# Performance work log

Measured on AMD Instinct MI355X. Metric: run time of the kernel, lower is better.

The kernel has to match this reference:

```python
import jax, jax.numpy as jnp
import numpy as np

N_NODES = 50000
HID = 256


def _gcn_norm(edge_index, n_nodes):
    # PyG GCNConv default: add self-loops, symmetric normalization
    src, dst = edge_index[0], edge_index[1]
    loop = jnp.arange(n_nodes, dtype=src.dtype)
    src = jnp.concatenate([src, loop])
    dst = jnp.concatenate([dst, loop])
    deg = jax.ops.segment_sum(jnp.ones_like(src, dtype=jnp.float32), dst, num_segments=n_nodes)
    dinv = jnp.where(deg > 0, jax.lax.rsqrt(jnp.maximum(deg, 1.0)), 0.0)
    norm = dinv[src] * dinv[dst]  # [E + N]
    return src, dst, norm


def _gcn_conv(x, W, b, src, dst, norm, n_nodes):
    h = x @ W                                   # [N, H] dense transform first (PyG order)
    msg = h[src] * norm[:, None]                # gather + scale
    out = jax.ops.segment_sum(msg, dst, num_segments=n_nodes)
    return out + b


def setup_inputs() -> dict:
    key = jax.random.key(0)
    ks = jax.random.split(key, 8)
    x = jax.random.normal(ks[0], (N_NODES, HID), dtype=jnp.float32)
    edge_index = jax.random.randint(ks[1], (2, 1600000), 0, N_NODES, dtype=jnp.int64)
    s = 1.0 / np.sqrt(HID)
    W1 = jax.random.normal(ks[2], (HID, HID), dtype=jnp.float32) * s
    b1 = jnp.zeros((HID,), dtype=jnp.float32)
    Wmu = jax.random.normal(ks[3], (HID, HID), dtype=jnp.float32) * s
    bmu = jnp.zeros((HID,), dtype=jnp.float32)
    Wls = jax.random.normal(ks[4], (HID, HID), dtype=jnp.float32) * s * 0.1
    bls = jnp.zeros((HID,), dtype=jnp.float32)
    return {"x": x, "edge_index": edge_index, "W1": W1, "b1": b1,
            "Wmu": Wmu, "bmu": bmu, "Wls": Wls, "bls": bls}


def reference(x, edge_index, W1, b1, Wmu, bmu, Wls, bls):
    n = x.shape[0]
    src, dst, norm = _gcn_norm(edge_index, n)
    h = jax.nn.relu(_gcn_conv(x, W1, b1, src, dst, norm, n))
    mu = _gcn_conv(h, Wmu, bmu, src, dst, norm, n)
    logstd = _gcn_conv(h, Wls, bls, src, dst, norm, n)
    std = jnp.exp(logstd)
    eps = jax.random.normal(jax.random.key(1), std.shape, dtype=std.dtype)
    z = mu + std * eps
    return (z, mu, logstd)
```

## Files before the change

### kernel.cpp

```cpp
#include <hip/hip_runtime.h>
#include <stdint.h>

#define HID 256

typedef __bf16 bf16x8 __attribute__((ext_vector_type(8)));
typedef float  f32x4  __attribute__((ext_vector_type(4)));
typedef unsigned int uint4v __attribute__((ext_vector_type(4)));

__device__ __forceinline__ unsigned short f2bf(float f){
  unsigned int x = __float_as_uint(f);
  x += 0x7FFFu + ((x >> 16) & 1u);
  return (unsigned short)(x >> 16);
}
__device__ __forceinline__ float bf2f(unsigned int u){
  return __uint_as_float(u << 16);
}
__device__ __forceinline__ float bflo(unsigned int x){ return __uint_as_float(x << 16); }
__device__ __forceinline__ float bfhi(unsigned int x){ return __uint_as_float(x & 0xFFFF0000u); }
__device__ __forceinline__ bf16x8 ntload8(const unsigned short* p){
  uint4v t = __builtin_nontemporal_load((const uint4v*)p);
  return __builtin_bit_cast(bf16x8, t);
}

__global__ void count_kernel(const int* __restrict__ ei, int E, int* __restrict__ deg){
  int e = blockIdx.x*256 + threadIdx.x;
  if (e < E) atomicAdd(&deg[ei[E + e]], 1);
}

__global__ void dinv_kernel(const int* __restrict__ deg, float* __restrict__ dinv, int N){
  int i = blockIdx.x*256 + threadIdx.x;
  if (i < N) dinv[i] = 1.0f / sqrtf((float)(deg[i] + 1));
}

__global__ void scan1_kernel(const int* __restrict__ deg, int* __restrict__ rowptr,
                             int* __restrict__ partials, int N){
  __shared__ int sm[256];
  int t = threadIdx.x;
  int i = blockIdx.x*256 + t;
  int v = (i < N) ? deg[i] : 0;
  int acc = v;
  sm[t] = acc;
  __syncthreads();
  for (int off = 1; off < 256; off <<= 1){
    int add = (t >= off) ? sm[t - off] : 0;
    __syncthreads();
    acc += add;
    sm[t] = acc;
    __syncthreads();
  }
  if (i < N) rowptr[i] = acc - v;
  if (t == 255) partials[blockIdx.x] = acc;
}

__global__ void scan2_kernel(int* __restrict__ partials, int nb){
  __shared__ int sm[256];
  int t = threadIdx.x;
  int v = (t < nb) ? partials[t] : 0;
  int acc = v;
  sm[t] = acc;
  __syncthreads();
  for (int off = 1; off < 256; off <<= 1){
    int add = (t >= off) ? sm[t - off] : 0;
    __syncthreads();
    acc += add;
    sm[t] = acc;
    __syncthreads();
  }
  if (t < nb) partials[t] = acc - v;
}

__global__ void scan3_kernel(int* __restrict__ rowptr, const int* __restrict__ partials,
                             int N, int E){
  int i = blockIdx.x*256 + threadIdx.x;
  if (i < N) rowptr[i] += partials[blockIdx.x];
  if (i == 0) rowptr[N] = E;
}

__global__ void scatter_kernel(const int* __restrict__ ei, int E, const int* __restrict__ rowptr,
                               int* __restrict__ fill, const float* __restrict__ dinv,
                               int* __restrict__ col, float* __restrict__ wgt){
  int e = blockIdx.x*256 + threadIdx.x;
  if (e >= E) return;
  int s = ei[e];
  int d = ei[E + e];
  int p = rowptr[d] + atomicAdd(&fill[d], 1);
  col[p] = s;
  wgt[p] = dinv[s] * dinv[d];
}

__global__ void convX_kernel(const float* __restrict__ x, unsigned short* __restrict__ xb, int total8){
  int t = blockIdx.x*256 + threadIdx.x;
  if (t >= total8) return;
  const float* p = x + (size_t)t*8;
  f32x4 a = *(const f32x4*)p;
  f32x4 b = *(const f32x4*)(p + 4);
  ushort4 o0, o1;
  o0.x = f2bf(a[0]); o0.y = f2bf(a[1]); o0.z = f2bf(a[2]); o0.w = f2bf(a[3]);
  o1.x = f2bf(b[0]); o1.y = f2bf(b[1]); o1.z = f2bf(b[2]); o1.w = f2bf(b[3]);
  ushort4* q = (ushort4*)(xb + (size_t)t*8);
  q[0] = o0; q[1] = o1;
}

__global__ void convW_kernel(const float* __restrict__ W1, const float* __restrict__ Wmu,
                             const float* __restrict__ Wls, unsigned short* __restrict__ Wt){
  int t = blockIdx.x*256 + threadIdx.x;
  if (t >= 3*65536) return;
  int m = t >> 16;
  int r = t & 0xFFFF;
  int n = r >> 8, k = r & 255;
  int ksrc = (m == 0) ? k : ((k & ~63) | ((k & 3) << 4) | ((k >> 2) & 15));
  const float* W = (m == 0) ? W1 : (m == 1 ? Wmu : Wls);
  Wt[t] = f2bf(W[ksrc*HID + n]);
}

__global__ void agg_bf16(const unsigned short* __restrict__ X, unsigned short* __restrict__ Y,
                         const int* __restrict__ rowptr, const int* __restrict__ col,
                         const float* __restrict__ wgt, const float* __restrict__ dinv,
                         int N, int sin, int sout){
  int w = (blockIdx.x * blockDim.x + threadIdx.x) >> 6;
  int lane = threadIdx.x & 63;
  if (w >= N) return;
  int q  = lane >> 4;
  int cl = lane & 15;
  float acc[16];
  #pragma unroll
  for (int k = 0; k < 16; ++k) acc[k] = 0.f;
  int p0 = rowptr[w], p1 = rowptr[w+1];
  for (int base = p0; base < p1; base += 64){
    int idx = base + lane;
    int sc = 0; float wc = 0.f;
    if (idx < p1){ sc = col[idx]; wc = wgt[idx]; }
    int cnt = min(p1 - base, 64);
    for (int j = 0; j < cnt; j += 4){
      int   s = __shfl(sc, j + q);
      float f = __shfl(wc, j + q);
      const unsigned short* rp = X + (size_t)s*sin + cl*16;
      uint4v u0 = *(const uint4v*)rp;
      uint4v u1 = *(const uint4v*)(rp + 8);
      acc[ 0]=fmaf(bflo(u0.x),f,acc[ 0]); acc[ 1]=fmaf(bfhi(u0.x),f,acc[ 1]);
      acc[ 2]=fmaf(bflo(u0.y),f,acc[ 2]); acc[ 3]=fmaf(bfhi(u0.y),f,acc[ 3]);
      acc[ 4]=fmaf(bflo(u0.z),f,acc[ 4]); acc[ 5]=fmaf(bfhi(u0.z),f,acc[ 5]);
      acc[ 6]=fmaf(bflo(u0.w),f,acc[ 6]); acc[ 7]=fmaf(bfhi(u0.w),f,acc[ 7]);
      acc[ 8]=fmaf(bflo(u1.x),f,acc[ 8]); acc[ 9]=fmaf(bfhi(u1.x),f,acc[ 9]);
      acc[10]=fmaf(bflo(u1.y),f,acc[10]); acc[11]=fmaf(bfhi(u1.y),f,acc[11]);
      acc[12]=fmaf(bflo(u1.z),f,acc[12]); acc[13]=fmaf(bfhi(u1.z),f,acc[13]);
      acc[14]=fmaf(bflo(u1.w),f,acc[14]); acc[15]=fmaf(bfhi(u1.w),f,acc[15]);
    }
  }
  #pragma unroll
  for (int k = 0; k < 16; ++k){
    acc[k] += __shfl_xor(acc[k], 16);
    acc[k] += __shfl_xor(acc[k], 32);
  }
  if (q == 0){
    float s2 = dinv[w]; s2 *= s2;
    const unsigned short* rp = X + (size_t)w*sin + cl*16;
    uint4v u0 = *(const uint4v*)rp;
    uint4v u1 = *(const uint4v*)(rp + 8);
    acc[ 0]=fmaf(bflo(u0.x),s2,acc[ 0]); acc[ 1]=fmaf(bfhi(u0.x),s2,acc[ 1]);
    acc[ 2]=fmaf(bflo(u0.y),s2,acc[ 2]); acc[ 3]=fmaf(bfhi(u0.y),s2,acc[ 3]);
    acc[ 4]=fmaf(bflo(u0.z),s2,acc[ 4]); acc[ 5]=fmaf(bfhi(u0.z),s2,acc[ 5]);
    acc[ 6]=fmaf(bflo(u0.w),s2,acc[ 6]); acc[ 7]=fmaf(bfhi(u0.w),s2,acc[ 7]);
    acc[ 8]=fmaf(bflo(u1.x),s2,acc[ 8]); acc[ 9]=fmaf(bfhi(u1.x),s2,acc[ 9]);
    acc[10]=fmaf(bflo(u1.y),s2,acc[10]); acc[11]=fmaf(bfhi(u1.y),s2,acc[11]);
    acc[12]=fmaf(bflo(u1.z),s2,acc[12]); acc[13]=fmaf(bfhi(u1.z),s2,acc[13]);
    acc[14]=fmaf(bflo(u1.w),s2,acc[14]); acc[15]=fmaf(bfhi(u1.w),s2,acc[15]);
    uint4v o0, o1;
    o0.x = (unsigned int)f2bf(acc[ 0]) | ((unsigned int)f2bf(acc[ 1]) << 16);
    o0.y = (unsigned int)f2bf(acc[ 2]) | ((unsigned int)f2bf(acc[ 3]) << 16);
    o0.z = (unsigned int)f2bf(acc[ 4]) | ((unsigned int)f2bf(acc[ 5]) << 16);
    o0.w = (unsigned int)f2bf(acc[ 6]) | ((unsigned int)f2bf(acc[ 7]) << 16);
    o1.x = (unsigned int)f2bf(acc[ 8]) | ((unsigned int)f2bf(acc[ 9]) << 16);
    o1.y = (unsigned int)f2bf(acc[10]) | ((unsigned int)f2bf(acc[11]) << 16);
    o1.z = (unsigned int)f2bf(acc[12]) | ((unsigned int)f2bf(acc[13]) << 16);
    o1.w = (unsigned int)f2bf(acc[14]) | ((unsigned int)f2bf(acc[15]) << 16);
    uint4v* yp = (uint4v*)(Y + (size_t)w*sout + cl*16);
    yp[0] = o0; yp[1] = o1;
  }
}

__global__ __launch_bounds__(256, 8) void gemm1_kernel(const unsigned short* __restrict__ A,
    const unsigned short* __restrict__ Bt, const float* __restrict__ bias,
    unsigned short* __restrict__ H, int N){
  int r0 = blockIdx.x * 32;
  int lane = threadIdx.x & 63;
  int nw = threadIdx.x >> 6;
  int lr = lane & 15, kg = lane >> 4;
  f32x4 acc[2][4] = {};
  for (int ks = 0; ks < 8; ++ks){
    int kb = ks*32 + kg*8;
    bf16x8 af[2];
    #pragma unroll
    for (int rf = 0; rf < 2; ++rf){
      int row = r0 + rf*16 + lr; if (row > N-1) row = N-1;
      af[rf] = *(const bf16x8*)(A + (size_t)row*HID + kb);
    }
    #pragma unroll
    for (int cf = 0; cf < 4; ++cf){
      int c = nw*64 + cf*16 + lr;
      bf16x8 bfr = *(const bf16x8*)(Bt + (size_t)c*HID + kb);
      acc[0][cf] = __builtin_amdgcn_mfma_f32_16x16x32_bf16(af[0], bfr, acc[0][cf], 0, 0, 0);
      acc[1][cf] = __builtin_amdgcn_mfma_f32_16x16x32_bf16(af[1], bfr, acc[1][cf], 0, 0, 0);
    }
  }
  float bv[4];
  #pragma unroll
  for (int cf = 0; cf < 4; ++cf) bv[cf] = bias[nw*64 + cf*16 + lr];
  #pragma unroll
  for (int rf = 0; rf < 2; ++rf){
    #pragma unroll
    for (int i = 0; i < 4; ++i){
      int row = r0 + rf*16 + kg*4 + i;
      if (row < N){
        ushort4 o;
        o.x = f2bf(fmaxf(acc[rf][0][i] + bv[0], 0.0f));
        o.y = f2bf(fmaxf(acc[rf][1][i] + bv[1], 0.0f));
        o.z = f2bf(fmaxf(acc[rf][2][i] + bv[2], 0.0f));
        o.w = f2bf(fmaxf(acc[rf][3][i] + bv[3], 0.0f));
        *(ushort4*)(H + (size_t)row*HID + nw*64 + lr*4) = o;
      }
    }
  }
}

__device__ __forceinline__ unsigned int rotl32(unsigned int v, int r){
  return (v << r) | (v >> (32 - r));
}

__device__ __forceinline__ float gauss_eps(unsigned int idxv){
  unsigned int x0 = 0u, x1 = idxv;
  const unsigned int ks0 = 0u, ks1 = 1u, ks2 = 0x1BD11BDAu ^ 0u ^ 1u;
  x0 += ks0; x1 += ks1;
#define TFR(r) { x0 += x1; x1 = rotl32(x1, r); x1 ^= x0; }
  TFR(13) TFR(15) TFR(26) TFR(6)   x0 += ks1; x1 += ks2 + 1u;
  TFR(17) TFR(29) TFR(16) TFR(24)  x0 += ks2; x1 += ks0 + 2u;
  TFR(13) TFR(15) TFR(26) TFR(6)   x0 += ks0; x1 += ks1 + 3u;
  TFR(17) TFR(29) TFR(16) TFR(24)  x0 += ks1; x1 += ks2 + 4u;
  TFR(13) TFR(15) TFR(26) TFR(6)   x0 += ks2; x1 += ks0 + 5u;
#undef TFR
  unsigned int bits = x0 ^ x1;
  float f = __uint_as_float((bits >> 9) | 0x3F800000u) - 1.0f;
  const float lo = -0.99999994f;
  float u = fmaxf(lo, fmaf(f, 2.0f, lo));
  float t = fmaf(-u, u, 1.0f);
  float wv = -0.69314718056f * __builtin_amdgcn_logf(t);
  float p;
  if (wv < 5.0f){
    wv -= 2.5f;
    p = 2.81022636e-08f;
    p = fmaf(p, wv, 3.43273939e-07f);
    p = fmaf(p, wv, -3.5233877e-06f);
    p = fmaf(p, wv, -4.39150654e-06f);
    p = fmaf(p, wv, 0.00021858087f);
    p = fmaf(p, wv, -0.00125372503f);
    p = fmaf(p, wv, -0.00417768164f);
    p = fmaf(p, wv, 0.246640727f);
    p = fmaf(p, wv, 1.50140941f);
  } else {
    wv = sqrtf(wv) - 3.0f;
    p = -0.000200214257f;
    p = fmaf(p, wv, 0.000100950558f);
    p = fmaf(p, wv, 0.00134934322f);
    p = fmaf(p, wv, -0.00367342844f);
    p = fmaf(p, wv, 0.00573950773f);
    p = fmaf(p, wv, -0.0076224613f);
    p = fmaf(p, wv, 0.00943887047f);
    p = fmaf(p, wv, 1.00167406f);
    p = fmaf(p, wv, 2.83297682f);
  }
  return 1.4142135381698608f * (p * u);
}

__global__ __launch_bounds__(256, 5) void gemm2_kernel(const unsigned short* __restrict__ A2b,
    const unsigned short* __restrict__ Bt, const float* __restrict__ bias,
    float* __restrict__ OUT, int N, int sa){
  __shared__ float sml[16][260];
  int r0 = blockIdx.x * 32;
  int lane = threadIdx.x & 63;
  int nw = threadIdx.x >> 6;
  int lr = lane & 15, kg = lane >> 4;
  f32x4 acc[2][4] = {};
  for (int ks = 0; ks < 8; ++ks){
    int kb = ks*32 + kg*8;
    bf16x8 af[2];
    #pragma unroll
    for (int rf = 0; rf < 2; ++rf){
      int row = r0 + rf*16 + lr; if (row > N-1) row = N-1;
      af[rf] = ntload8(A2b + (size_t)row*sa + kb);
    }
    #pragma unroll
    for (int cf = 0; cf < 4; ++cf){
      int c = nw*64 + cf*16 + lr;
      bf16x8 bfr = *(const bf16x8*)(Bt + (size_t)c*HID + kb);
      acc[0][cf] = __builtin_amdgcn_mfma_f32_16x16x32_bf16(af[0], bfr, acc[0][cf], 0, 0, 0);
      acc[1][cf] = __builtin_amdgcn_mfma_f32_16x16x32_bf16(af[1], bfr, acc[1][cf], 0, 0, 0);
    }
  }
  f32x4 b4 = *(const f32x4*)(bias + lane*4);
  for (int rf = 0; rf < 2; ++rf){
    #pragma unroll
    for (int cf = 0; cf < 4; ++cf){
      int c = nw*64 + cf*16 + lr;
      #pragma unroll
      for (int i = 0; i < 4; ++i) sml[kg*4 + i][c] = acc[rf][cf][i];
    }
    __syncthreads();
    #pragma unroll
    for (int rr = 0; rr < 4; ++rr){
      int rl = nw*4 + rr;
      int row = r0 + rf*16 + rl;
      if (row < N){
        f32x4 m4 = *(const f32x4*)&sml[rl][lane*4];
        m4 += b4;
        __builtin_nontemporal_store(m4, (f32x4*)(OUT + (size_t)row*HID + lane*4));
      }
    }
    __syncthreads();
  }
}

__global__ __launch_bounds__(256, 5) void gemm3_kernel(const unsigned short* __restrict__ A2b,
    const unsigned short* __restrict__ Bt, const float* __restrict__ bias,
    const float* __restrict__ MU, float* __restrict__ Z, float* __restrict__ LS, int N, int sa){
  __shared__ float sml[16][260];
  int r0 = blockIdx.x * 32;
  int lane = threadIdx.x & 63;
  int nw = threadIdx.x >> 6;
  int lr = lane & 15, kg = lane >> 4;
  f32x4 acc[2][4] = {};
  for (int ks = 0; ks < 8; ++ks){
    int kb = ks*32 + kg*8;
    bf16x8 af[2];
    #pragma unroll
    for (int rf = 0; rf < 2; ++rf){
      int row = r0 + rf*16 + lr; if (row > N-1) row = N-1;
      af[rf] = ntload8(A2b + (size_t)row*sa + kb);
    }
    #pragma unroll
    for (int cf = 0; cf < 4; ++cf){
      int c = nw*64 + cf*16 + lr;
      bf16x8 bfr = *(const bf16x8*)(Bt + (size_t)c*HID + kb);
      acc[0][cf] = __builtin_amdgcn_mfma_f32_16x16x32_bf16(af[0], bfr, acc[0][cf], 0, 0, 0);
      acc[1][cf] = __builtin_amdgcn_mfma_f32_16x16x32_bf16(af[1], bfr, acc[1][cf], 0, 0, 0);
    }
  }
  f32x4 b4 = *(const f32x4*)(bias + lane*4);
  for (int rf = 0; rf < 2; ++rf){
    #pragma unroll
    for (int cf = 0; cf < 4; ++cf){
      int c = nw*64 + cf*16 + lr;
      #pragma unroll
      for (int i = 0; i < 4; ++i) sml[kg*4 + i][c] = acc[rf][cf][i];
    }
    __syncthreads();
    #pragma unroll
    for (int rr = 0; rr < 4; ++rr){
      int rl = nw*4 + rr;
      int row = r0 + rf*16 + rl;
      if (row < N){
        size_t base = (size_t)row*HID + lane*4;
        f32x4 l4 = *(const f32x4*)&sml[rl][lane*4];
        l4 += b4;
        f32x4 m4 = *(const f32x4*)(MU + base);
        f32x4 z4;
        #pragma unroll
        for (int j = 0; j < 4; ++j){
          float e = gauss_eps((unsigned int)(base + j));
          float s = __builtin_amdgcn_exp2f(l4[j] * 1.44269504f);
          z4[j] = fmaf(s, e, m4[j]);
        }
        __builtin_nontemporal_store(z4, (f32x4*)(Z  + base));
        __builtin_nontemporal_store(l4, (f32x4*)(LS + base));
      }
    }
    __syncthreads();
  }
}

extern "C" void kernel_launch(void* const* d_in, const int* in_sizes, int n_in,
                              void* d_out, int out_size, void* d_ws, size_t ws_size,
                              hipStream_t stream){
  const float* x   = (const float*)d_in[0];
  const int*   ei  = (const int*)d_in[1];
  const float* W1  = (const float*)d_in[2];
  const float* b1  = (const float*)d_in[3];
  const float* Wmu = (const float*)d_in[4];
  const float* bmu = (const float*)d_in[5];
  const float* Wls = (const float*)d_in[6];
  const float* bls = (const float*)d_in[7];
  const int N = in_sizes[0] / HID;
  const int E = in_sizes[1] / 2;
  const size_t NA = ((size_t)N + 64) & ~(size_t)63;

  int* deg      = (int*)d_ws;
  int* fill     = deg + NA;
  int* rowptr   = fill + NA;
  int* partials = rowptr + NA;
  float* dinv   = (float*)(partials + 1024);
  int*  col     = (int*)(dinv + NA);
  float* wgt    = (float*)(col + (size_t)E);
  unsigned short* Wt = (unsigned short*)(wgt + (size_t)E);
  unsigned short* a2ws = Wt + 3*65536;

  float* Z  = (float*)d_out;
  float* MU = Z + (size_t)N*HID;
  float* LS = MU + (size_t)N*HID;
  unsigned short* hb  = (unsigned short*)Z;
  unsigned short* xb  = (unsigned short*)Z + (size_t)N*HID;
  unsigned short* a1b = (unsigned short*)MU;

  size_t ws_used = (size_t)((char*)a2ws - (char*)d_ws);
  bool packed = (ws_size >= ws_used + (size_t)N * 256 * sizeof(unsigned short));
  unsigned short* a2b = packed ? a2ws : (unsigned short*)LS;
  int sa = packed ? 256 : 512;

  hipMemsetAsync(deg, 0, NA*2*sizeof(int), stream);

  int ebl = (E + 255)/256, nbl = (N + 255)/256;
  count_kernel  <<<ebl, 256, 0, stream>>>(ei, E, deg);
  dinv_kernel   <<<nbl, 256, 0, stream>>>(deg, dinv, N);
  scan1_kernel  <<<nbl, 256, 0, stream>>>(deg, rowptr, partials, N);
  scan2_kernel  <<<1,   256, 0, stream>>>(partials, nbl);
  scan3_kernel  <<<nbl, 256, 0, stream>>>(rowptr, partials, N, E);
  scatter_kernel<<<ebl, 256, 0, stream>>>(ei, E, rowptr, fill, dinv, col, wgt);
  convW_kernel  <<<768, 256, 0, stream>>>(W1, Wmu, Wls, Wt);
  convX_kernel  <<<(N*HID/8 + 255)/256, 256, 0, stream>>>(x, xb, N*HID/8);

  agg_bf16    <<<(N + 3)/4,  256, 0, stream>>>(xb, a1b, rowptr, col, wgt, dinv, N, 256, 256);
  gemm1_kernel<<<(N + 31)/32, 256, 0, stream>>>(a1b, Wt, b1, hb, N);
  agg_bf16    <<<(N + 3)/4,  256, 0, stream>>>(hb, a2b, rowptr, col, wgt, dinv, N, 256, sa);
  gemm2_kernel<<<(N + 31)/32, 256, 0, stream>>>(a2b, Wt + 65536,   bmu, MU, N, sa);
  gemm3_kernel<<<(N + 31)/32, 256, 0, stream>>>(a2b, Wt + 2*65536, bls, MU, Z, LS, N, sa);
}
```

Before: 761.7 us.

## Fuse setup kernels, interleave edge col/weight, prefetch edges in aggregation

Folds the dinv computation into the first scan kernel and merges the W and X bf16 conversion kernels into one launch, cutting two launches. Packs column index and edge weight into one int2 array so the scatter writes and the aggregation reads a single 8-byte record per edge. The aggregation loop now loads the next 64-edge chunk before processing the current one, so the edge fetch overlaps the gathers. The MU read in gemm3 uses a nontemporal load. Each piece is small and the launch savings are only a few microseconds.

```diff
diff --git a/kernel.cpp b/kernel.cpp
--- a/kernel.cpp
+++ b/kernel.cpp
@@ -6,14 +6,12 @@
 typedef __bf16 bf16x8 __attribute__((ext_vector_type(8)));
 typedef float  f32x4  __attribute__((ext_vector_type(4)));
 typedef unsigned int uint4v __attribute__((ext_vector_type(4)));
+typedef unsigned int uint2v __attribute__((ext_vector_type(2)));
 
 __device__ __forceinline__ unsigned short f2bf(float f){
   unsigned int x = __float_as_uint(f);
   x += 0x7FFFu + ((x >> 16) & 1u);
   return (unsigned short)(x >> 16);
-}
-__device__ __forceinline__ float bf2f(unsigned int u){
-  return __uint_as_float(u << 16);
 }
 __device__ __forceinline__ float bflo(unsigned int x){ return __uint_as_float(x << 16); }
 __device__ __forceinline__ float bfhi(unsigned int x){ return __uint_as_float(x & 0xFFFF0000u); }
@@ -27,17 +25,13 @@
   if (e < E) atomicAdd(&deg[ei[E + e]], 1);
 }
 
-__global__ void dinv_kernel(const int* __restrict__ deg, float* __restrict__ dinv, int N){
-  int i = blockIdx.x*256 + threadIdx.x;
-  if (i < N) dinv[i] = 1.0f / sqrtf((float)(deg[i] + 1));
-}
-
 __global__ void scan1_kernel(const int* __restrict__ deg, int* __restrict__ rowptr,
-                             int* __restrict__ partials, int N){
+                             int* __restrict__ partials, float* __restrict__ dinv, int N){
   __shared__ int sm[256];
   int t = threadIdx.x;
   int i = blockIdx.x*256 + t;
   int v = (i < N) ? deg[i] : 0;
+  if (i < N) dinv[i] = 1.0f / sqrtf((float)(v + 1));
   int acc = v;
   sm[t] = acc;
   __syncthreads();
@@ -78,18 +72,31 @@
 
 __global__ void scatter_kernel(const int* __restrict__ ei, int E, const int* __restrict__ rowptr,
                                int* __restrict__ fill, const float* __restrict__ dinv,
-                               int* __restrict__ col, float* __restrict__ wgt){
+                               int2* __restrict__ ew){
   int e = blockIdx.x*256 + threadIdx.x;
   if (e >= E) return;
   int s = ei[e];
   int d = ei[E + e];
   int p = rowptr[d] + atomicAdd(&fill[d], 1);
-  col[p] = s;
-  wgt[p] = dinv[s] * dinv[d];
-}
-
-__global__ void convX_kernel(const float* __restrict__ x, unsigned short* __restrict__ xb, int total8){
+  int2 v; v.x = s; v.y = __float_as_int(dinv[s] * dinv[d]);
+  ew[p] = v;
+}
+
+__global__ void convWX_kernel(const float* __restrict__ W1, const float* __restrict__ Wmu,
+                              const float* __restrict__ Wls, unsigned short* __restrict__ Wt,
+                              const float* __restrict__ x, unsigned short* __restrict__ xb,
+                              int total8){
   int t = blockIdx.x*256 + threadIdx.x;
+  if (t < 3*65536){
+    int m = t >> 16;
+    int r = t & 0xFFFF;
+    int n = r >> 8, k = r & 255;
+    int ksrc = (m == 0) ? k : ((k & ~63) | ((k & 3) << 4) | ((k >> 2) & 15));
+    const float* W = (m == 0) ? W1 : (m == 1 ? Wmu : Wls);
+    Wt[t] = f2bf(W[ksrc*HID + n]);
+    return;
+  }
+  t -= 3*65536;
   if (t >= total8) return;
   const float* p = x + (size_t)t*8;
   f32x4 a = *(const f32x4*)p;
@@ -97,26 +104,13 @@
   ushort4 o0, o1;
   o0.x = f2bf(a[0]); o0.y = f2bf(a[1]); o0.z = f2bf(a[2]); o0.w = f2bf(a[3]);
   o1.x = f2bf(b[0]); o1.y = f2bf(b[1]); o1.z = f2bf(b[2]); o1.w = f2bf(b[3]);
-  ushort4* q = (ushort4*)(xb + (size_t)t*8);
-  q[0] = o0; q[1] = o1;
-}
-
-__global__ void convW_kernel(const float* __restrict__ W1, const float* __restrict__ Wmu,
-                             const float* __restrict__ Wls, unsigned short* __restrict__ Wt){
-  int t = blockIdx.x*256 + threadIdx.x;
-  if (t >= 3*65536) return;
-  int m = t >> 16;
-  int r = t & 0xFFFF;
-  int n = r >> 8, k = r & 255;
-  int ksrc = (m == 0) ? k : ((k & ~63) | ((k & 3) << 4) | ((k >> 2) & 15));
-  const float* W = (m == 0) ? W1 : (m == 1 ? Wmu : Wls);
-  Wt[t] = f2bf(W[ksrc*HID + n]);
+  ushort4* qq = (ushort4*)(xb + (size_t)t*8);
+  qq[0] = o0; qq[1] = o1;
 }
 
 __global__ void agg_bf16(const unsigned short* __restrict__ X, unsigned short* __restrict__ Y,
-                         const int* __restrict__ rowptr, const int* __restrict__ col,
-                         const float* __restrict__ wgt, const float* __restrict__ dinv,
-                         int N, int sin, int sout){
+                         const int* __restrict__ rowptr, const int2* __restrict__ ew,
+                         const float* __restrict__ dinv, int N, int sin, int sout){
   int w = (blockIdx.x * blockDim.x + threadIdx.x) >> 6;
   int lane = threadIdx.x & 63;
   if (w >= N) return;
@@ -126,14 +120,22 @@
   #pragma unroll
   for (int k = 0; k < 16; ++k) acc[k] = 0.f;
   int p0 = rowptr[w], p1 = rowptr[w+1];
+  int sc = 0; float wc = 0.f;
+  {
+    int idx = p0 + lane;
+    if (idx < p1){ uint2v e = __builtin_nontemporal_load((const uint2v*)(ew + idx));
+                   sc = (int)e.x; wc = __uint_as_float(e.y); }
+  }
   for (int base = p0; base < p1; base += 64){
-    int idx = base + lane;
-    int sc = 0; float wc = 0.f;
-    if (idx < p1){ sc = col[idx]; wc = wgt[idx]; }
+    int cur_s = sc; float cur_w = wc;
+    sc = 0; wc = 0.f;
+    int nidx = base + 64 + lane;
+    if (nidx < p1){ uint2v e = __builtin_nontemporal_load((const uint2v*)(ew + nidx));
+                    sc = (int)e.x; wc = __uint_as_float(e.y); }
     int cnt = min(p1 - base, 64);
     for (int j = 0; j < cnt; j += 4){
-      int   s = __shfl(sc, j + q);
-      float f = __shfl(wc, j + q);
+      int   s = __shfl(cur_s, j + q);
+      float f = __shfl(cur_w, j + q);
       const unsigned short* rp = X + (size_t)s*sin + cl*16;
       uint4v u0 = *(const uint4v*)rp;
       uint4v u1 = *(const uint4v*)(rp + 8);
@@ -321,7 +323,8 @@
 
 __global__ __launch_bounds__(256, 5) void gemm3_kernel(const unsigned short* __restrict__ A2b,
     const unsigned short* __restrict__ Bt, const float* __restrict__ bias,
-    const float* __restrict__ MU, float* __restrict__ Z, float* __restrict__ LS, int N, int sa){
+    const float* __restrict__ MU, float* __restrict__ Z, float* __restrict__ LS,
+    int N, int sa){
   __shared__ float sml[16][260];
   int r0 = blockIdx.x * 32;
   int lane = threadIdx.x & 63;
@@ -361,7 +364,7 @@
         size_t base = (size_t)row*HID + lane*4;
         f32x4 l4 = *(const f32x4*)&sml[rl][lane*4];
         l4 += b4;
-        f32x4 m4 = *(const f32x4*)(MU + base);
+        f32x4 m4 = __builtin_nontemporal_load((const f32x4*)(MU + base));
         f32x4 z4;
         #pragma unroll
         for (int j = 0; j < 4; ++j){
@@ -397,9 +400,8 @@
   int* rowptr   = fill + NA;
   int* partials = rowptr + NA;
   float* dinv   = (float*)(partials + 1024);
-  int*  col     = (int*)(dinv + NA);
-  float* wgt    = (float*)(col + (size_t)E);
-  unsigned short* Wt = (unsigned short*)(wgt + (size_t)E);
+  int2* ew      = (int2*)(dinv + NA);
+  unsigned short* Wt = (unsigned short*)(ew + (size_t)E);
   unsigned short* a2ws = Wt + 3*65536;
 
   float* Z  = (float*)d_out;
@@ -417,18 +419,17 @@
   hipMemsetAsync(deg, 0, NA*2*sizeof(int), stream);
 
   int ebl = (E + 255)/256, nbl = (N + 255)/256;
+  int total8 = N*HID/8;
   count_kernel  <<<ebl, 256, 0, stream>>>(ei, E, deg);
-  dinv_kernel   <<<nbl, 256, 0, stream>>>(deg, dinv, N);
-  scan1_kernel  <<<nbl, 256, 0, stream>>>(deg, rowptr, partials, N);
+  scan1_kernel  <<<nbl, 256, 0, stream>>>(deg, rowptr, partials, dinv, N);
   scan2_kernel  <<<1,   256, 0, stream>>>(partials, nbl);
   scan3_kernel  <<<nbl, 256, 0, stream>>>(rowptr, partials, N, E);
-  scatter_kernel<<<ebl, 256, 0, stream>>>(ei, E, rowptr, fill, dinv, col, wgt);
-  convW_kernel  <<<768, 256, 0, stream>>>(W1, Wmu, Wls, Wt);
-  convX_kernel  <<<(N*HID/8 + 255)/256, 256, 0, stream>>>(x, xb, N*HID/8);
-
-  agg_bf16    <<<(N + 3)/4,  256, 0, stream>>>(xb, a1b, rowptr, col, wgt, dinv, N, 256, 256);
+  scatter_kernel<<<ebl, 256, 0, stream>>>(ei, E, rowptr, fill, dinv, ew);
+  convWX_kernel <<<(3*65536 + total8 + 255)/256, 256, 0, stream>>>(W1, Wmu, Wls, Wt, x, xb, total8);
+
+  agg_bf16    <<<(N + 3)/4,  256, 0, stream>>>(xb, a1b, rowptr, ew, dinv, N, 256, 256);
   gemm1_kernel<<<(N + 31)/32, 256, 0, stream>>>(a1b, Wt, b1, hb, N);
-  agg_bf16    <<<(N + 3)/4,  256, 0, stream>>>(hb, a2b, rowptr, col, wgt, dinv, N, 256, sa);
+  agg_bf16    <<<(N + 3)/4,  256, 0, stream>>>(hb, a2b, rowptr, ew, dinv, N, 256, sa);
   gemm2_kernel<<<(N + 31)/32, 256, 0, stream>>>(a2b, Wt + 65536,   bmu, MU, N, sa);
   gemm3_kernel<<<(N + 31)/32, 256, 0, stream>>>(a2b, Wt + 2*65536, bls, MU, Z, LS, N, sa);
 }
```

Result: faster. 730.3 us (-4.1%).
